# Kernel optimization log

Measured on AMD Instinct MI355X. Metric: run time of the kernel, lower is better.

## Reference

```python
import jax, jax.numpy as jnp
import numpy as np

B, S, HID = 1, 2048, 4096
NH, NKV, HD = 32, 8, 128
N_REP = NH // NKV
SCALING = HD ** -0.5
NEG_INF = jnp.float32(-jnp.inf)


def rotate_half(x):
    x1, x2 = jnp.split(x, 2, axis=-1)
    return jnp.concatenate((-x2, x1), axis=-1)


def setup_inputs() -> dict:
    key = jax.random.key(0)
    ks = jax.random.split(key, 8)
    hidden_states = jax.random.normal(ks[0], (B, S, HID), dtype=jnp.float32)
    # RoPE tables (uniform stand-ins; real cos/sin come from rotary embedding)
    pos = jnp.arange(S, dtype=jnp.float32)[:, None]
    inv_freq = 1.0 / (10000.0 ** (jnp.arange(0, HD, 2, dtype=jnp.float32) / HD))
    ang = pos * inv_freq[None, :]              # [S, HD/2]
    emb = jnp.concatenate([ang, ang], axis=-1)  # [S, HD]
    cos = jnp.cos(emb)[None].repeat(B, axis=0)  # [B, S, HD]
    sin = jnp.sin(emb)[None].repeat(B, axis=0)
    # HF-style additive causal mask: 0 on/below diagonal, -inf above
    tril = jnp.tril(jnp.ones((S, S), dtype=bool))
    attention_mask = jnp.where(tril, 0.0, NEG_INF).astype(jnp.float32)[None, None]  # [B,1,S,S]
    scale = 0.02
    q_w = jax.random.normal(ks[1], (HID, HID), dtype=jnp.float32) * scale
    k_w = jax.random.normal(ks[2], (NKV * HD, HID), dtype=jnp.float32) * scale
    v_w = jax.random.normal(ks[3], (NKV * HD, HID), dtype=jnp.float32) * scale
    o_w = jax.random.normal(ks[4], (HID, HID), dtype=jnp.float32) * scale
    return {"hidden_states": hidden_states, "cos": cos, "sin": sin,
            "attention_mask": attention_mask, "q_w": q_w, "k_w": k_w,
            "v_w": v_w, "o_w": o_w}


def reference(hidden_states, cos, sin, attention_mask, q_w, k_w, v_w, o_w):
    b, s, _ = hidden_states.shape
    # projections -> [B, H, S, D]
    q = (hidden_states @ q_w.T).reshape(b, s, NH, HD).transpose(0, 2, 1, 3)
    k = (hidden_states @ k_w.T).reshape(b, s, NKV, HD).transpose(0, 2, 1, 3)
    v = (hidden_states @ v_w.T).reshape(b, s, NKV, HD).transpose(0, 2, 1, 3)
    # RoPE (unsqueeze_dim=1)
    cos_u = cos[:, None, :, :]
    sin_u = sin[:, None, :, :]
    q = q * cos_u + rotate_half(q) * sin_u
    k = k * cos_u + rotate_half(k) * sin_u
    # repeat_kv (interleave each kv head n_rep times)
    k = jnp.repeat(k, N_REP, axis=1)
    v = jnp.repeat(v, N_REP, axis=1)
    attn = jnp.einsum("bhqd,bhkd->bhqk", q, k)
    # gen_mask: 0 -> 1, -inf -> 0 (passthrough otherwise)
    m = attention_mask
    mask01 = jnp.where(m == 0, 1.0, jnp.where(jnp.isneginf(m), 0.0, m))
    attn = attn * mask01
    causal = m[:, :, :, : k.shape[-2]]
    attn = (attn + causal) * SCALING
    probs = jax.nn.softmax(attn.astype(jnp.float32), axis=-1).astype(q.dtype)
    # dropout p=attention_dropout=0.0 in eval -> identity
    ctx = jnp.einsum("bhqk,bhkd->bhqd", probs, v)  # [B,H,S,D]
    out = ctx.transpose(0, 2, 1, 3).reshape(b, s, -1) @ o_w.T
    return out
```

## Files before the change

kernel.cpp:

```cpp
#include <hip/hip_runtime.h>


typedef __attribute__((ext_vector_type(8))) short bf16x8;
typedef __attribute__((ext_vector_type(4))) float f32x4;
typedef __attribute__((ext_vector_type(4))) unsigned short u16x4;

#define S_LEN 2048
#define HID 4096
#define NH 32
#define NKV 8
#define HD 128
#define KVDIM 1024
#define SCALING 0.08838834764831845f
#define ASC 0.12751744f
#define THR2 11.5415603f

__device__ inline unsigned short f2bf(float f) {
  unsigned u = __builtin_bit_cast(unsigned, f);
  u = (u + 0x7FFFu + ((u >> 16) & 1u)) >> 16;
  return (unsigned short)u;
}
__device__ inline unsigned short f2bf_fast(float f) {
  unsigned u = __builtin_bit_cast(unsigned, f);
  return (unsigned short)((u + 0x8000u) >> 16);
}
__device__ inline float bf2f(unsigned short h) {
  unsigned u = ((unsigned)h) << 16;
  return __builtin_bit_cast(float, u);
}

__device__ inline void gload_lds16(const unsigned short* g, unsigned short* l) {
  __builtin_amdgcn_global_load_lds(
      (const __attribute__((address_space(1))) void*)g,
      (__attribute__((address_space(3))) void*)l, 16, 0, 0);
}

#define SZ_HS (8388608u)
#define SZ_QW (16777216u)
#define SZ_KW (4194304u)
#define B0 SZ_HS
#define B1 (B0 + SZ_QW)
#define B2 (B1 + SZ_KW)
#define B3 (B2 + SZ_KW)
#define B4 (B3 + SZ_QW)

__global__ void cvt_all(const float* __restrict__ s0,
                        const float* __restrict__ s1,
                        const float* __restrict__ s2,
                        const float* __restrict__ s3,
                        const float* __restrict__ s4,
                        unsigned short* __restrict__ dst) {
  size_t i = ((size_t)blockIdx.x * blockDim.x + threadIdx.x) * 4;
  const float* src;
  size_t off;
  if (i < B0)      { src = s0; off = i; }
  else if (i < B1) { src = s1; off = i - B0; }
  else if (i < B2) { src = s2; off = i - B1; }
  else if (i < B3) { src = s3; off = i - B2; }
  else             { src = s4; off = i - B3; }
  f32x4 v = *(const f32x4*)(src + off);
  u16x4 o;
#pragma unroll
  for (int r = 0; r < 4; ++r) o[r] = f2bf(v[r]);
  *(u16x4*)(dst + i) = o;
}

__global__ __launch_bounds__(256, 3) void gemm_qkv(
    const unsigned short* __restrict__ A, const unsigned short* __restrict__ Bq_,
    const unsigned short* __restrict__ Bk_, const unsigned short* __restrict__ Bv_,
    const float* __restrict__ cosb, const float* __restrict__ sinb,
    unsigned short* __restrict__ Cq, unsigned short* __restrict__ Ck,
    unsigned short* __restrict__ Cvt) {
  __shared__ unsigned short As[2][128 * 32];
  __shared__ unsigned short Bs[2][128 * 32];
  const int K = HID;
  const int tid = threadIdx.x;
  const int lane = tid & 63;
  const int wave = tid >> 6;
  const int orig = blockIdx.y * gridDim.x + blockIdx.x;
  const int xcd = orig & 7, seq = orig >> 3;
  const int xt = xcd * ((int)gridDim.x >> 3) + (seq >> 4);
  const int yt = seq & 15;
  const int m0 = yt * 128;
  const int wr = wave >> 1, wc = wave & 1;
  const int lrow = lane & 15, lg = lane >> 4;

  const unsigned short* Bsel;
  if (xt < 32)      Bsel = Bq_ + (size_t)(xt * 128) * K;
  else if (xt < 40) Bsel = Bk_ + (size_t)((xt - 32) * 128) * K;
  else              Bsel = Bv_ + (size_t)((xt - 40) * 128) * K;

  const f32x4 zero = {0.f, 0.f, 0.f, 0.f};
  f32x4 acc[4][4];
#pragma unroll
  for (int i = 0; i < 4; ++i)
#pragma unroll
    for (int j = 0; j < 4; ++j) acc[i][j] = zero;

  const int r0s = tid >> 2, c0s = (tid & 3) * 8;
  const int r1s = (tid + 256) >> 2, c1s = ((tid + 256) & 3) * 8;
  const unsigned short* Ag0 = A + (size_t)(m0 + r0s) * K + c0s;
  const unsigned short* Ag1 = A + (size_t)(m0 + r1s) * K + c1s;
  const unsigned short* Bg0 = Bsel + (size_t)r0s * K + c0s;
  const unsigned short* Bg1 = Bsel + (size_t)r1s * K + c1s;
  unsigned short* Al0[2] = {&As[0][tid * 8], &As[1][tid * 8]};
  unsigned short* Al1[2] = {&As[0][(tid + 256) * 8], &As[1][(tid + 256) * 8]};
  unsigned short* Bl0[2] = {&Bs[0][tid * 8], &Bs[1][tid * 8]};
  unsigned short* Bl1[2] = {&Bs[0][(tid + 256) * 8], &Bs[1][(tid + 256) * 8]};

#define QKV_STAGE(buf, koff)                                                  \
  {                                                                           \
    gload_lds16(Ag0 + (koff), Al0[buf]);                                      \
    gload_lds16(Ag1 + (koff), Al1[buf]);                                      \
    gload_lds16(Bg0 + (koff), Bl0[buf]);                                      \
    gload_lds16(Bg1 + (koff), Bl1[buf]);                                      \
  }

  int colb[4];
#pragma unroll
  for (int j = 0; j < 4; ++j)
    colb[j] = wc * 32 + (j & 1) * 16 + (j >> 1) * 64;

  QKV_STAGE(0, 0);
  __syncthreads();
  int cur = 0;
  const int NT = K >> 5;
  for (int kt = 0; kt < NT; ++kt) {
    if (kt + 1 < NT) QKV_STAGE(cur ^ 1, (kt + 1) * 32);
    bf16x8 af[4], bq[4];
#pragma unroll
    for (int i = 0; i < 4; ++i)
      af[i] = *(const bf16x8*)(&As[cur][(wr * 64 + i * 16 + lrow) * 32 + lg * 8]);
#pragma unroll
    for (int j = 0; j < 4; ++j)
      bq[j] = *(const bf16x8*)(&Bs[cur][(colb[j] + lrow) * 32 + lg * 8]);
#pragma unroll
    for (int i = 0; i < 4; ++i)
#pragma unroll
      for (int j = 0; j < 4; ++j)
        acc[i][j] = __builtin_amdgcn_mfma_f32_16x16x32_bf16(af[i], bq[j],
                                                            acc[i][j], 0, 0, 0);
    __syncthreads();
    cur ^= 1;
  }
#undef QKV_STAGE

  if (xt < 40) {
    unsigned short* C = (xt < 32) ? Cq : Ck;
    const int ldc = (xt < 32) ? HID : KVDIM;
    const int n0 = (xt < 32) ? xt * 128 : (xt - 32) * 128;
#pragma unroll
    for (int i = 0; i < 4; ++i) {
#pragma unroll
      for (int jp = 0; jp < 2; ++jp) {
        const int d64 = wc * 32 + jp * 16 + lrow;
#pragma unroll
        for (int r = 0; r < 4; ++r) {
          const int s = m0 + wr * 64 + i * 16 + lg * 4 + r;
          const float cv = cosb[(size_t)s * 128 + d64];
          const float sv = sinb[(size_t)s * 128 + d64];
          const float lo = acc[i][jp][r], hi = acc[i][jp + 2][r];
          C[(size_t)s * ldc + n0 + d64]      = f2bf(lo * cv - hi * sv);
          C[(size_t)s * ldc + n0 + d64 + 64] = f2bf(hi * cv + lo * sv);
        }
      }
    }
  } else {
    const int n0 = (xt - 40) * 128;
#pragma unroll
    for (int i = 0; i < 4; ++i)
#pragma unroll
      for (int j = 0; j < 4; ++j) {
        const int mm = m0 + wr * 64 + i * 16 + lg * 4;
        const int nn = n0 + colb[j] + lrow;
        u16x4 pk;
#pragma unroll
        for (int r = 0; r < 4; ++r) pk[r] = f2bf(acc[i][j][r]);
        *(u16x4*)(Cvt + (size_t)nn * S_LEN + mm) = pk;
      }
  }
}

__global__ __launch_bounds__(256, 3) void gemm_o(
    const unsigned short* __restrict__ A, const unsigned short* __restrict__ B,
    float* __restrict__ C) {
  __shared__ unsigned short As[2][128 * 32];
  __shared__ unsigned short Bs[2][128 * 32];
  const int K = HID;
  const int tid = threadIdx.x;
  const int lane = tid & 63;
  const int wave = tid >> 6;
  const int orig = blockIdx.y * gridDim.x + blockIdx.x;
  const int xcd = orig & 7, seq = orig >> 3;
  const int xt = xcd * ((int)gridDim.x >> 3) + (seq >> 4);
  const int yt = seq & 15;
  const int m0 = yt * 128;
  const int n0 = xt * 128;
  const int wr = wave >> 1, wc = wave & 1;
  const int lrow = lane & 15, lg = lane >> 4;

  const f32x4 zero = {0.f, 0.f, 0.f, 0.f};
  f32x4 acc[4][4];
#pragma unroll
  for (int i = 0; i < 4; ++i)
#pragma unroll
    for (int j = 0; j < 4; ++j) acc[i][j] = zero;

  const int r0s = tid >> 2, c0s = (tid & 3) * 8;
  const int r1s = (tid + 256) >> 2, c1s = ((tid + 256) & 3) * 8;
  const unsigned short* Ag0 = A + (size_t)(m0 + r0s) * K + c0s;
  const unsigned short* Ag1 = A + (size_t)(m0 + r1s) * K + c1s;
  const unsigned short* Bg0 = B + (size_t)(n0 + r0s) * K + c0s;
  const unsigned short* Bg1 = B + (size_t)(n0 + r1s) * K + c1s;
  unsigned short* Al0[2] = {&As[0][tid * 8], &As[1][tid * 8]};
  unsigned short* Al1[2] = {&As[0][(tid + 256) * 8], &As[1][(tid + 256) * 8]};
  unsigned short* Bl0[2] = {&Bs[0][tid * 8], &Bs[1][tid * 8]};
  unsigned short* Bl1[2] = {&Bs[0][(tid + 256) * 8], &Bs[1][(tid + 256) * 8]};

#define O_STAGE(buf, koff)                                                    \
  {                                                                           \
    gload_lds16(Ag0 + (koff), Al0[buf]);                                      \
    gload_lds16(Ag1 + (koff), Al1[buf]);                                      \
    gload_lds16(Bg0 + (koff), Bl0[buf]);                                      \
    gload_lds16(Bg1 + (koff), Bl1[buf]);                                      \
  }

  O_STAGE(0, 0);
  __syncthreads();
  int cur = 0;
  const int NT = K >> 5;
  for (int kt = 0; kt < NT; ++kt) {
    if (kt + 1 < NT) O_STAGE(cur ^ 1, (kt + 1) * 32);
    bf16x8 af[4], bq[4];
#pragma unroll
    for (int i = 0; i < 4; ++i) {
      af[i] = *(const bf16x8*)(&As[cur][(wr * 64 + i * 16 + lrow) * 32 + lg * 8]);
      bq[i] = *(const bf16x8*)(&Bs[cur][(wc * 64 + i * 16 + lrow) * 32 + lg * 8]);
    }
#pragma unroll
    for (int i = 0; i < 4; ++i)
#pragma unroll
      for (int j = 0; j < 4; ++j)
        acc[i][j] = __builtin_amdgcn_mfma_f32_16x16x32_bf16(af[i], bq[j],
                                                            acc[i][j], 0, 0, 0);
    __syncthreads();
    cur ^= 1;
  }
#undef O_STAGE

#pragma unroll
  for (int i = 0; i < 4; ++i)
#pragma unroll
    for (int j = 0; j < 4; ++j) {
      const int mm = m0 + wr * 64 + i * 16 + lg * 4;
      const int nn = n0 + wc * 64 + j * 16 + lrow;
#pragma unroll
      for (int r = 0; r < 4; ++r)
        C[(size_t)(mm + r) * HID + nn] = acc[i][j][r];
    }
}

__global__ __launch_bounds__(256, 2) void attn_kernel(
    const unsigned short* __restrict__ Q, const unsigned short* __restrict__ Kc,
    const unsigned short* __restrict__ Vt, unsigned short* __restrict__ ctx) {
  __shared__ unsigned short Ks[2][64 * 128];
  __shared__ unsigned short Vs[2][128 * 64];
  __shared__ unsigned short Ps[4][16 * 72];
  const int tid = threadIdx.x;
  const int lane = tid & 63;
  const int wave = tid >> 6;
  const int h = blockIdx.x;
  const int hk = h >> 2;
  const int yl = (int)gridDim.y - 1 - blockIdx.y;
  const int r0 = yl * 64 + wave * 16;
  const int lrow = lane & 15, lg = lane >> 4;

  bf16x8 aq[4];
  {
    const unsigned short* qb =
        Q + (size_t)(r0 + lrow) * HID + h * HD + lg * 8;
#pragma unroll
    for (int kk = 0; kk < 4; ++kk) aq[kk] = *(const bf16x8*)(qb + kk * 32);
  }

  const f32x4 zero = {0.f, 0.f, 0.f, 0.f};
  f32x4 o[8];
#pragma unroll
  for (int t = 0; t < 8; ++t) o[t] = zero;
  float l_i = 0.f;
  float m_i = -1e30f;

  const unsigned short* Kg[4];
  const unsigned short* Vg[4];
  int Koff[4], Voff[4];
#pragma unroll
  for (int qq = 0; qq < 4; ++qq) {
    const int slot = tid + 256 * qq;
    {
      const int row = slot >> 4, ch = slot & 15;
      Kg[qq] = Kc + (size_t)row * KVDIM + hk * HD + ((ch ^ (row & 7)) * 8);
      Koff[qq] = slot * 8;
    }
    {
      const int row = slot >> 3, ch = slot & 7;
      Vg[qq] = Vt + ((size_t)hk * HD + row) * S_LEN + ((ch ^ (row & 7)) * 8);
      Voff[qq] = slot * 8;
    }
  }
  unsigned short* pw = &Ps[wave][0];

#pragma unroll
  for (int qq = 0; qq < 4; ++qq) gload_lds16(Kg[qq], &Ks[0][Koff[qq]]);
#pragma unroll
  for (int qq = 0; qq < 4; ++qq) gload_lds16(Vg[qq], &Vs[0][Voff[qq]]);
  __syncthreads();

  const int NTk = yl + 1;
  for (int t = 0; t < NTk; ++t) {
    const int k0 = t << 6;
    const int cur = t & 1;
    const bool pf = (t + 1 < NTk);
    if (pf) {
#pragma unroll
      for (int qq = 0; qq < 4; ++qq)
        gload_lds16(Kg[qq] + (size_t)(k0 + 64) * KVDIM, &Ks[cur ^ 1][Koff[qq]]);
    }

    const bool compute = (k0 <= r0 + 15);
    f32x4 sacc[4];
    if (compute) {
#pragma unroll
      for (int c = 0; c < 4; ++c) sacc[c] = zero;
      __builtin_amdgcn_s_setprio(1);
#pragma unroll
      for (int c = 0; c < 4; ++c) {
        const int krow = c * 16 + lrow;
        bf16x8 bk[4];
#pragma unroll
        for (int kk = 0; kk < 4; ++kk)
          bk[kk] = *(const bf16x8*)(&Ks[cur][krow * 128 +
                                            (((kk * 4 + lg) ^ (krow & 7)) * 8)]);
#pragma unroll
        for (int kk = 0; kk < 4; ++kk)
          sacc[c] = __builtin_amdgcn_mfma_f32_16x16x32_bf16(
              bk[kk], aq[kk], sacc[c], 0, 0, 0);
      }
      __builtin_amdgcn_s_setprio(0);
    }
    if (pf) {
#pragma unroll
      for (int qq = 0; qq < 4; ++qq)
        gload_lds16(Vg[qq] + (k0 + 64), &Vs[cur ^ 1][Voff[qq]]);
    }
    if (compute) {
      const bool full = (k0 + 63 <= r0);
      const int q = r0 + lrow;
#pragma unroll
      for (int c = 0; c < 4; ++c)
#pragma unroll
        for (int r = 0; r < 4; ++r) {
          float v = sacc[c][r] * ASC;
          if (!full) {
            const int k = k0 + c * 16 + lg * 4 + r;
            v = (k <= q) ? v : -1e30f;
          }
          sacc[c][r] = v;
        }
      float m0v = fmaxf(fmaxf(sacc[0][0], sacc[0][1]),
                        fmaxf(sacc[0][2], sacc[0][3]));
      float m1v = fmaxf(fmaxf(sacc[1][0], sacc[1][1]),
                        fmaxf(sacc[1][2], sacc[1][3]));
      float m2v = fmaxf(fmaxf(sacc[2][0], sacc[2][1]),
                        fmaxf(sacc[2][2], sacc[2][3]));
      float m3v = fmaxf(fmaxf(sacc[3][0], sacc[3][1]),
                        fmaxf(sacc[3][2], sacc[3][3]));
      float tv = fmaxf(fmaxf(m0v, m1v), fmaxf(m2v, m3v));
      tv = fmaxf(tv, __shfl_xor(tv, 16, 64));
      tv = fmaxf(tv, __shfl_xor(tv, 32, 64));
      const float tm = tv;
      const bool grow = (tm > m_i + THR2);
      if (__any(grow)) {
        const float mn = fmaxf(m_i, tm);
        const float scq = __builtin_amdgcn_exp2f(m_i - mn);
        m_i = mn;
        l_i *= scq;
#pragma unroll
        for (int r = 0; r < 4; ++r) {
          const float scD = __shfl(scq, lg * 4 + r, 64);
#pragma unroll
          for (int t2 = 0; t2 < 8; ++t2) o[t2][r] *= scD;
        }
      }
      bf16x8 pa[2];
      {
        float rs = 0.f;
#pragma unroll
        for (int c = 0; c < 4; ++c) {
          u16x4 pk;
#pragma unroll
          for (int r = 0; r < 4; ++r) {
            const float p = __builtin_amdgcn_exp2f(sacc[c][r] - m_i);
            rs += p;
            pk[r] = f2bf_fast(p);
          }
          *(u16x4*)(pw + lrow * 72 + c * 16 + lg * 4) = pk;
        }
        rs += __shfl_xor(rs, 16, 64);
        rs += __shfl_xor(rs, 32, 64);
        l_i += rs;
#pragma unroll
        for (int ks = 0; ks < 2; ++ks)
          pa[ks] = *(const bf16x8*)(pw + lrow * 72 + ks * 32 + lg * 8);
      }
      __builtin_amdgcn_s_setprio(1);
#pragma unroll
      for (int t2 = 0; t2 < 8; ++t2) {
        const int vrow = t2 * 16 + lrow;
#pragma unroll
        for (int ks = 0; ks < 2; ++ks) {
          bf16x8 bv = *(const bf16x8*)(&Vs[cur][vrow * 64 +
                                               (((ks * 4 + lg) ^ (vrow & 7)) * 8)]);
          o[t2] = __builtin_amdgcn_mfma_f32_16x16x32_bf16(pa[ks], bv,
                                                          o[t2], 0, 0, 0);
        }
      }
      __builtin_amdgcn_s_setprio(0);
    }
    __syncthreads();
  }
  const float inv1 = 1.f / l_i;
#pragma unroll
  for (int r = 0; r < 4; ++r) {
    const float invD = __shfl(inv1, lg * 4 + r, 64);
#pragma unroll
    for (int t = 0; t < 8; ++t)
      ctx[(size_t)(r0 + lg * 4 + r) * HID + h * HD + t * 16 + lrow] =
          f2bf(o[t][r] * invD);
  }
}

extern "C" void kernel_launch(void* const* d_in, const int* in_sizes, int n_in,
                              void* d_out, int out_size, void* d_ws,
                              size_t ws_size, hipStream_t stream) {
  (void)in_sizes; (void)n_in; (void)out_size; (void)ws_size;
  const float* hs   = (const float*)d_in[0];
  const float* cosb = (const float*)d_in[1];
  const float* sinb = (const float*)d_in[2];
  const float* qw = (const float*)d_in[4];
  const float* kw = (const float*)d_in[5];
  const float* vw = (const float*)d_in[6];
  const float* ow = (const float*)d_in[7];
  float* out = (float*)d_out;

  unsigned short* ws = (unsigned short*)d_ws;
  unsigned short* hs_b = ws;
  unsigned short* qw_b = hs_b + SZ_HS;
  unsigned short* kw_b = qw_b + SZ_QW;
  unsigned short* vw_b = kw_b + SZ_KW;
  unsigned short* ow_b = vw_b + SZ_KW;
  unsigned short* q_b  = ow_b + SZ_QW;
  unsigned short* k_b  = q_b + SZ_HS;
  unsigned short* vt_b = k_b + (size_t)S_LEN * KVDIM;
  unsigned short* ctx_b = vt_b + (size_t)KVDIM * S_LEN;

  cvt_all<<<B4 / 1024, 256, 0, stream>>>(hs, qw, kw, vw, ow, hs_b);

  gemm_qkv<<<dim3(48, 16), 256, 0, stream>>>(hs_b, qw_b, kw_b, vw_b,
                                             cosb, sinb, q_b, k_b, vt_b);

  attn_kernel<<<dim3(NH, S_LEN / 64), 256, 0, stream>>>(q_b, k_b, vt_b, ctx_b);

  gemm_o<<<dim3(32, 16), 256, 0, stream>>>(ctx_b, ow_b, out);
}
```

Measured before the change: 329.1 us.

## Swizzle GEMM LDS tiles and overlap o_w conversion with attention

Both GEMMs now load global data into LDS with an XOR-swizzled row/chunk mapping, and the fragment reads use the matching swizzled offset. This is meant to remove LDS bank conflicts on the MFMA operand reads. The o_w fp32-to-bf16 conversion is taken out of the upfront conversion kernel and done by 128 extra blocks appended to the attention grid. Those blocks run alongside the causal attention tail, which is load-imbalanced, at the cost of competing for bandwidth and CUs.

```diff
diff --git a/kernel.cpp b/kernel.cpp
--- a/kernel.cpp
+++ b/kernel.cpp
@@ -42,13 +42,11 @@
 #define B1 (B0 + SZ_QW)
 #define B2 (B1 + SZ_KW)
 #define B3 (B2 + SZ_KW)
-#define B4 (B3 + SZ_QW)
 
 __global__ void cvt_all(const float* __restrict__ s0,
                         const float* __restrict__ s1,
                         const float* __restrict__ s2,
                         const float* __restrict__ s3,
-                        const float* __restrict__ s4,
                         unsigned short* __restrict__ dst) {
   size_t i = ((size_t)blockIdx.x * blockDim.x + threadIdx.x) * 4;
   const float* src;
@@ -56,13 +54,18 @@
   if (i < B0)      { src = s0; off = i; }
   else if (i < B1) { src = s1; off = i - B0; }
   else if (i < B2) { src = s2; off = i - B1; }
-  else if (i < B3) { src = s3; off = i - B2; }
-  else             { src = s4; off = i - B3; }
+  else             { src = s3; off = i - B2; }
   f32x4 v = *(const f32x4*)(src + off);
   u16x4 o;
 #pragma unroll
   for (int r = 0; r < 4; ++r) o[r] = f2bf(v[r]);
   *(u16x4*)(dst + i) = o;
+}
+
+__device__ inline const unsigned short* swz_src(const unsigned short* base,
+                                                int s, int K) {
+  const int g = s >> 3, q = s & 7, ls = q ^ (g & 7);
+  return base + (size_t)(2 * g + (ls >> 2)) * K + (ls & 3) * 8;
 }
 
 __global__ __launch_bounds__(256, 3) void gemm_qkv(
@@ -97,12 +100,10 @@
 #pragma unroll
     for (int j = 0; j < 4; ++j) acc[i][j] = zero;
 
-  const int r0s = tid >> 2, c0s = (tid & 3) * 8;
-  const int r1s = (tid + 256) >> 2, c1s = ((tid + 256) & 3) * 8;
-  const unsigned short* Ag0 = A + (size_t)(m0 + r0s) * K + c0s;
-  const unsigned short* Ag1 = A + (size_t)(m0 + r1s) * K + c1s;
-  const unsigned short* Bg0 = Bsel + (size_t)r0s * K + c0s;
-  const unsigned short* Bg1 = Bsel + (size_t)r1s * K + c1s;
+  const unsigned short* Ag0 = swz_src(A + (size_t)m0 * K, tid, K);
+  const unsigned short* Ag1 = swz_src(A + (size_t)m0 * K, tid + 256, K);
+  const unsigned short* Bg0 = swz_src(Bsel, tid, K);
+  const unsigned short* Bg1 = swz_src(Bsel, tid + 256, K);
   unsigned short* Al0[2] = {&As[0][tid * 8], &As[1][tid * 8]};
   unsigned short* Al1[2] = {&As[0][(tid + 256) * 8], &As[1][(tid + 256) * 8]};
   unsigned short* Bl0[2] = {&Bs[0][tid * 8], &Bs[1][tid * 8]};
@@ -120,6 +121,9 @@
 #pragma unroll
   for (int j = 0; j < 4; ++j)
     colb[j] = wc * 32 + (j & 1) * 16 + (j >> 1) * 64;
+
+  const int gl = lrow >> 1, p = lrow & 1;
+  const int psw = gl * 64 + ((((p << 2) | lg) ^ (gl & 7)) << 3);
 
   QKV_STAGE(0, 0);
   __syncthreads();
@@ -130,10 +134,10 @@
     bf16x8 af[4], bq[4];
 #pragma unroll
     for (int i = 0; i < 4; ++i)
-      af[i] = *(const bf16x8*)(&As[cur][(wr * 64 + i * 16 + lrow) * 32 + lg * 8]);
+      af[i] = *(const bf16x8*)(&As[cur][(wr * 64 + i * 16) * 32 + psw]);
 #pragma unroll
     for (int j = 0; j < 4; ++j)
-      bq[j] = *(const bf16x8*)(&Bs[cur][(colb[j] + lrow) * 32 + lg * 8]);
+      bq[j] = *(const bf16x8*)(&Bs[cur][colb[j] * 32 + psw]);
 #pragma unroll
     for (int i = 0; i < 4; ++i)
 #pragma unroll
@@ -206,12 +210,10 @@
 #pragma unroll
     for (int j = 0; j < 4; ++j) acc[i][j] = zero;
 
-  const int r0s = tid >> 2, c0s = (tid & 3) * 8;
-  const int r1s = (tid + 256) >> 2, c1s = ((tid + 256) & 3) * 8;
-  const unsigned short* Ag0 = A + (size_t)(m0 + r0s) * K + c0s;
-  const unsigned short* Ag1 = A + (size_t)(m0 + r1s) * K + c1s;
-  const unsigned short* Bg0 = B + (size_t)(n0 + r0s) * K + c0s;
-  const unsigned short* Bg1 = B + (size_t)(n0 + r1s) * K + c1s;
+  const unsigned short* Ag0 = swz_src(A + (size_t)m0 * K, tid, K);
+  const unsigned short* Ag1 = swz_src(A + (size_t)m0 * K, tid + 256, K);
+  const unsigned short* Bg0 = swz_src(B + (size_t)n0 * K, tid, K);
+  const unsigned short* Bg1 = swz_src(B + (size_t)n0 * K, tid + 256, K);
   unsigned short* Al0[2] = {&As[0][tid * 8], &As[1][tid * 8]};
   unsigned short* Al1[2] = {&As[0][(tid + 256) * 8], &As[1][(tid + 256) * 8]};
   unsigned short* Bl0[2] = {&Bs[0][tid * 8], &Bs[1][tid * 8]};
@@ -224,6 +226,9 @@
     gload_lds16(Bg0 + (koff), Bl0[buf]);                                      \
     gload_lds16(Bg1 + (koff), Bl1[buf]);                                      \
   }
+
+  const int gl = lrow >> 1, p = lrow & 1;
+  const int psw = gl * 64 + ((((p << 2) | lg) ^ (gl & 7)) << 3);
 
   O_STAGE(0, 0);
   __syncthreads();
@@ -234,8 +239,8 @@
     bf16x8 af[4], bq[4];
 #pragma unroll
     for (int i = 0; i < 4; ++i) {
-      af[i] = *(const bf16x8*)(&As[cur][(wr * 64 + i * 16 + lrow) * 32 + lg * 8]);
-      bq[i] = *(const bf16x8*)(&Bs[cur][(wc * 64 + i * 16 + lrow) * 32 + lg * 8]);
+      af[i] = *(const bf16x8*)(&As[cur][(wr * 64 + i * 16) * 32 + psw]);
+      bq[i] = *(const bf16x8*)(&Bs[cur][(wc * 64 + i * 16) * 32 + psw]);
     }
 #pragma unroll
     for (int i = 0; i < 4; ++i)
@@ -262,16 +267,32 @@
 
 __global__ __launch_bounds__(256, 2) void attn_kernel(
     const unsigned short* __restrict__ Q, const unsigned short* __restrict__ Kc,
-    const unsigned short* __restrict__ Vt, unsigned short* __restrict__ ctx) {
+    const unsigned short* __restrict__ Vt, unsigned short* __restrict__ ctx,
+    const float* __restrict__ ow, unsigned short* __restrict__ owb) {
   __shared__ unsigned short Ks[2][64 * 128];
   __shared__ unsigned short Vs[2][128 * 64];
   __shared__ unsigned short Ps[4][16 * 72];
   const int tid = threadIdx.x;
+
+  if (blockIdx.y >= 32) {
+    const int cb = (int)(blockIdx.y - 32) * 32 + blockIdx.x;
+    size_t idx = ((size_t)cb * 256 + tid) * 4;
+    const size_t stride = (size_t)128 * 256 * 4;
+    for (; idx < SZ_QW; idx += stride) {
+      f32x4 v = *(const f32x4*)(ow + idx);
+      u16x4 o;
+#pragma unroll
+      for (int r = 0; r < 4; ++r) o[r] = f2bf(v[r]);
+      *(u16x4*)(owb + idx) = o;
+    }
+    return;
+  }
+
   const int lane = tid & 63;
   const int wave = tid >> 6;
   const int h = blockIdx.x;
   const int hk = h >> 2;
-  const int yl = (int)gridDim.y - 1 - blockIdx.y;
+  const int yl = 31 - (int)blockIdx.y;
   const int r0 = yl * 64 + wave * 16;
   const int lrow = lane & 15, lg = lane >> 4;
 
@@ -399,9 +420,9 @@
           u16x4 pk;
 #pragma unroll
           for (int r = 0; r < 4; ++r) {
-            const float p = __builtin_amdgcn_exp2f(sacc[c][r] - m_i);
-            rs += p;
-            pk[r] = f2bf_fast(p);
+            const float p2 = __builtin_amdgcn_exp2f(sacc[c][r] - m_i);
+            rs += p2;
+            pk[r] = f2bf_fast(p2);
           }
           *(u16x4*)(pw + lrow * 72 + c * 16 + lg * 4) = pk;
         }
@@ -463,12 +484,13 @@
   unsigned short* vt_b = k_b + (size_t)S_LEN * KVDIM;
   unsigned short* ctx_b = vt_b + (size_t)KVDIM * S_LEN;
 
-  cvt_all<<<B4 / 1024, 256, 0, stream>>>(hs, qw, kw, vw, ow, hs_b);
+  cvt_all<<<B3 / 1024, 256, 0, stream>>>(hs, qw, kw, vw, hs_b);
 
   gemm_qkv<<<dim3(48, 16), 256, 0, stream>>>(hs_b, qw_b, kw_b, vw_b,
                                              cosb, sinb, q_b, k_b, vt_b);
 
-  attn_kernel<<<dim3(NH, S_LEN / 64), 256, 0, stream>>>(q_b, k_b, vt_b, ctx_b);
+  attn_kernel<<<dim3(NH, 36), 256, 0, stream>>>(q_b, k_b, vt_b, ctx_b,
+                                                ow, ow_b);
 
   gemm_o<<<dim3(32, 16), 256, 0, stream>>>(ctx_b, ow_b, out);
 }
```

Result: slower. 382.1 us (+16.1%).
